# Optimization experiments

Hardware: AMD Instinct MI355X
Metric: run time of the kernel (lower is better)

## Reference

```python
import jax, jax.numpy as jnp
import numpy as np

NUM_HEADS = 16
GROUP_NUM = 4
HIDDEN = 1024
HEAD_DIM = HIDDEN // NUM_HEADS
EPS = 1e-5


def layernorm(x, g, b):
    mu = jnp.mean(x, axis=-1, keepdims=True)
    var = jnp.var(x, axis=-1, keepdims=True)
    return (x - mu) * jax.lax.rsqrt(var + EPS) * g + b


def setup_inputs() -> dict:
    key = jax.random.key(0)
    ks = jax.random.split(key, 12)
    s = 0.02
    return {
        "hidden_state": jax.random.normal(ks[0], (2, 2048, HIDDEN), jnp.float32),
        "wq": jax.random.normal(ks[1], (HIDDEN, HIDDEN), jnp.float32) * s,
        "bq": jnp.zeros((HIDDEN,), jnp.float32),
        "wk": jax.random.normal(ks[2], (GROUP_NUM * HEAD_DIM, HIDDEN), jnp.float32) * s,
        "bk": jnp.zeros((GROUP_NUM * HEAD_DIM,), jnp.float32),
        "wv": jax.random.normal(ks[3], (GROUP_NUM * HEAD_DIM, HIDDEN), jnp.float32) * s,
        "bv": jnp.zeros((GROUP_NUM * HEAD_DIM,), jnp.float32),
        "wo": jax.random.normal(ks[4], (HIDDEN, HIDDEN), jnp.float32) * s,
        "bo": jnp.zeros((HIDDEN,), jnp.float32),
        "ln_g": jnp.ones((HIDDEN,), jnp.float32),
        "ln_b": jnp.zeros((HIDDEN,), jnp.float32),
        "w1": jax.random.normal(ks[5], (HIDDEN, HIDDEN), jnp.float32) * s,
        "b1": jnp.zeros((HIDDEN,), jnp.float32),
        "w2": jax.random.normal(ks[6], (HIDDEN, HIDDEN), jnp.float32) * s,
        "b2": jnp.zeros((HIDDEN,), jnp.float32),
        "fln_g": jnp.ones((HIDDEN,), jnp.float32),
        "fln_b": jnp.zeros((HIDDEN,), jnp.float32),
    }


def reference(hidden_state, wq, bq, wk, bk, wv, bv, wo, bo, ln_g, ln_b,
              w1, b1, w2, b2, fln_g, fln_b):
    B, S, H = hidden_state.shape
    hpg = NUM_HEADS // GROUP_NUM  # heads per KV group

    q = hidden_state @ wq.T + bq  # [B,S,H]
    k = hidden_state @ wk.T + bk  # [B,S,G*D]
    v = hidden_state @ wv.T + bv

    q = q.reshape(B, S, NUM_HEADS, HEAD_DIM).transpose(0, 2, 1, 3)      # [B,Hh,S,D]
    k = k.reshape(B, S, GROUP_NUM, HEAD_DIM).transpose(0, 2, 1, 3)      # [B,G,S,D]
    v = v.reshape(B, S, GROUP_NUM, HEAD_DIM).transpose(0, 2, 1, 3)
    # expand KV groups to full head count (consecutive repeat, matching torch expand+reshape)
    k = jnp.repeat(k, hpg, axis=1)  # [B,Hh,S,D]
    v = jnp.repeat(v, hpg, axis=1)

    scale = 1.0 / jnp.sqrt(jnp.float32(HEAD_DIM))
    scores = jnp.einsum('bhsd,bhtd->bhst', q, k) * scale  # [B,Hh,S,S]
    probs = jax.nn.softmax(scores, axis=-1)
    attn = jnp.einsum('bhst,bhtd->bhsd', probs, v)  # [B,Hh,S,D]

    # Faithful to source: transpose(-1,-2) then raw flat view to [B, S, Hh*D]
    attn = jnp.swapaxes(attn, -1, -2).reshape(B, -1, HEAD_DIM * NUM_HEADS)

    out = layernorm(hidden_state + attn @ wo.T + bo, ln_g, ln_b)
    ffn = out @ w1.T + b1
    ffn = jax.nn.relu(ffn) @ w2.T + b2
    return layernorm(out + ffn, fln_g, fln_b)
```

## Files before the change

### kernel.cpp

```cpp
#include <hip/hip_runtime.h>
#include <math.h>

#define HIDDEN 1024
#define SEQ 2048

typedef __attribute__((ext_vector_type(8))) short short8;
typedef __attribute__((ext_vector_type(4))) float f32x4;

__device__ __forceinline__ unsigned short f2bf(float x) {
  union { float f; unsigned u; } c; c.f = x;
  unsigned r = c.u + 0x7FFFu + ((c.u >> 16) & 1u);
  return (unsigned short)(r >> 16);
}
__device__ __forceinline__ float bf2f(unsigned short h) {
  union { unsigned u; float f; } c; c.u = ((unsigned)h) << 16;
  return c.f;
}

__device__ __forceinline__ void async_copy16(const void* g, void* l) {
  __builtin_amdgcn_global_load_lds(
      (const __attribute__((address_space(1))) unsigned int*)g,
      (__attribute__((address_space(3))) unsigned int*)l, 16, 0, 0);
}

__global__ __launch_bounds__(256) void cvt_all(
    const float* __restrict__ hs, const float* __restrict__ wq,
    const float* __restrict__ wk, const float* __restrict__ wv,
    const float* __restrict__ wo, const float* __restrict__ w1,
    const float* __restrict__ w2,
    unsigned short* __restrict__ hsb, unsigned short* __restrict__ wqb,
    unsigned short* __restrict__ wkb, unsigned short* __restrict__ wvb,
    unsigned short* __restrict__ wob, unsigned short* __restrict__ w1b,
    unsigned short* __restrict__ w2b)
{
  const int i = blockIdx.x * 256 + threadIdx.x;
  const float* src; unsigned short* dst; int off;
  if (i < 1048576)      { src = hs; dst = hsb; off = i; }
  else if (i < 1310720) { src = wq; dst = wqb; off = i - 1048576; }
  else if (i < 1376256) { src = wk; dst = wkb; off = i - 1310720; }
  else if (i < 1441792) { src = wv; dst = wvb; off = i - 1376256; }
  else if (i < 1703936) { src = wo; dst = wob; off = i - 1441792; }
  else if (i < 1966080) { src = w1; dst = w1b; off = i - 1703936; }
  else                  { src = w2; dst = w2b; off = i - 1966080; }
  float4 v = ((const float4*)src)[off];
  ushort4 o;
  o.x = f2bf(v.x); o.y = f2bf(v.y); o.z = f2bf(v.z); o.w = f2bf(v.w);
  ((ushort4*)dst)[off] = o;
}

template<bool RELU>
__global__ __launch_bounds__(256) void gemm_mfma(
    const unsigned short* __restrict__ A, const unsigned short* __restrict__ W,
    const float* __restrict__ bias, unsigned short* __restrict__ C,
    int M, int N, int K)
{
  __shared__ unsigned short As[2][64 * 64];
  __shared__ unsigned short Bs[2][128 * 64];
  const int tid = threadIdx.x;
  const int lane = tid & 63, wave = tid >> 6;
  const int ln = lane & 15, quad = lane >> 4;
  const int wm = (wave >> 1) * 32, wn = (wave & 1) * 64;
  const int m0 = blockIdx.y * 64, n0 = blockIdx.x * 128;

  f32x4 acc[2][4];
#pragma unroll
  for (int i = 0; i < 2; ++i)
#pragma unroll
    for (int j = 0; j < 4; ++j) acc[i][j] = (f32x4){0.f, 0.f, 0.f, 0.f};

  auto stage = [&](int buf, int k0) {
#pragma unroll
    for (int it = 0; it < 2; ++it) {
      const int c = (wave * 2 + it) * 64 + lane;
      const int row = c >> 3, gc = (c & 7) ^ (row & 7);
      async_copy16(A + (size_t)(m0 + row) * K + k0 + gc * 8,
                   &As[buf][(wave * 2 + it) * 512]);
    }
#pragma unroll
    for (int it = 0; it < 4; ++it) {
      const int c = (wave * 4 + it) * 64 + lane;
      const int row = c >> 3, gc = (c & 7) ^ (row & 7);
      async_copy16(W + (size_t)(n0 + row) * K + k0 + gc * 8,
                   &Bs[buf][(wave * 4 + it) * 512]);
    }
  };

  stage(0, 0);
  for (int k0 = 0; k0 < K; k0 += 64) {
    const int buf = (k0 >> 6) & 1;
    __syncthreads();
    if (k0 + 64 < K) stage(buf ^ 1, k0 + 64);

    short8 af[2][2], bfr[4][2];
#pragma unroll
    for (int i = 0; i < 2; ++i) {
      const int row = wm + i * 16 + ln;
#pragma unroll
      for (int f = 0; f < 2; ++f) {
        const int ch = row * 8 + ((f * 4 + quad) ^ (row & 7));
        af[i][f] = *(const short8*)&As[buf][ch * 8];
      }
    }
#pragma unroll
    for (int j = 0; j < 4; ++j) {
      const int row = wn + j * 16 + ln;
#pragma unroll
      for (int f = 0; f < 2; ++f) {
        const int ch = row * 8 + ((f * 4 + quad) ^ (row & 7));
        bfr[j][f] = *(const short8*)&Bs[buf][ch * 8];
      }
    }
#pragma unroll
    for (int i = 0; i < 2; ++i)
#pragma unroll
      for (int j = 0; j < 4; ++j) {
        acc[i][j] = __builtin_amdgcn_mfma_f32_16x16x32_bf16(af[i][0], bfr[j][0], acc[i][j], 0, 0, 0);
        acc[i][j] = __builtin_amdgcn_mfma_f32_16x16x32_bf16(af[i][1], bfr[j][1], acc[i][j], 0, 0, 0);
      }
  }

#pragma unroll
  for (int j = 0; j < 4; ++j) {
    const int n = n0 + wn + j * 16 + ln;
    const float bv = bias[n];
#pragma unroll
    for (int i = 0; i < 2; ++i) {
#pragma unroll
      for (int rr = 0; rr < 4; ++rr) {
        const int m = m0 + wm + i * 16 + quad * 4 + rr;
        float v = acc[i][j][rr] + bv;
        if (RELU) v = fmaxf(v, 0.f);
        C[(size_t)m * N + n] = f2bf(v);
      }
    }
  }
}

__global__ __launch_bounds__(256) void gemm_qkv(
    const unsigned short* __restrict__ A,
    const unsigned short* __restrict__ Wq, const unsigned short* __restrict__ Wk,
    const unsigned short* __restrict__ Wv,
    const float* __restrict__ bq, const float* __restrict__ bk,
    const float* __restrict__ bv,
    unsigned short* __restrict__ Qo, unsigned short* __restrict__ Ko,
    unsigned short* __restrict__ Vt)
{
  __shared__ unsigned short As[2][64 * 64];
  __shared__ unsigned short Bs[2][128 * 64];
  const int bx = blockIdx.x;
  int mode, nw0;
  const unsigned short* W;
  const float* bias;
  if (bx < 8)       { mode = 0; W = Wq; bias = bq; nw0 = bx * 128; }
  else if (bx < 10) { mode = 1; W = Wk; bias = bk; nw0 = (bx - 8) * 128; }
  else              { mode = 2; W = Wv; bias = bv; nw0 = (bx - 10) * 128; }

  const int tid = threadIdx.x;
  const int lane = tid & 63, wave = tid >> 6;
  const int ln = lane & 15, quad = lane >> 4;
  const int wm = (wave >> 1) * 32, wn = (wave & 1) * 64;
  const int m0 = blockIdx.y * 64;
  const int K = 1024;

  f32x4 acc[2][4];
#pragma unroll
  for (int i = 0; i < 2; ++i)
#pragma unroll
    for (int j = 0; j < 4; ++j) acc[i][j] = (f32x4){0.f, 0.f, 0.f, 0.f};

  auto stage = [&](int buf, int k0) {
#pragma unroll
    for (int it = 0; it < 2; ++it) {
      const int c = (wave * 2 + it) * 64 + lane;
      const int row = c >> 3, gc = (c & 7) ^ (row & 7);
      async_copy16(A + (size_t)(m0 + row) * K + k0 + gc * 8,
                   &As[buf][(wave * 2 + it) * 512]);
    }
#pragma unroll
    for (int it = 0; it < 4; ++it) {
      const int c = (wave * 4 + it) * 64 + lane;
      const int row = c >> 3, gc = (c & 7) ^ (row & 7);
      async_copy16(W + (size_t)(nw0 + row) * K + k0 + gc * 8,
                   &Bs[buf][(wave * 4 + it) * 512]);
    }
  };

  stage(0, 0);
  for (int k0 = 0; k0 < K; k0 += 64) {
    const int buf = (k0 >> 6) & 1;
    __syncthreads();
    if (k0 + 64 < K) stage(buf ^ 1, k0 + 64);

    short8 af[2][2], bfr[4][2];
#pragma unroll
    for (int i = 0; i < 2; ++i) {
      const int row = wm + i * 16 + ln;
#pragma unroll
      for (int f = 0; f < 2; ++f) {
        const int ch = row * 8 + ((f * 4 + quad) ^ (row & 7));
        af[i][f] = *(const short8*)&As[buf][ch * 8];
      }
    }
#pragma unroll
    for (int j = 0; j < 4; ++j) {
      const int row = wn + j * 16 + ln;
#pragma unroll
      for (int f = 0; f < 2; ++f) {
        const int ch = row * 8 + ((f * 4 + quad) ^ (row & 7));
        bfr[j][f] = *(const short8*)&Bs[buf][ch * 8];
      }
    }
#pragma unroll
    for (int i = 0; i < 2; ++i)
#pragma unroll
      for (int j = 0; j < 4; ++j) {
        acc[i][j] = __builtin_amdgcn_mfma_f32_16x16x32_bf16(af[i][0], bfr[j][0], acc[i][j], 0, 0, 0);
        acc[i][j] = __builtin_amdgcn_mfma_f32_16x16x32_bf16(af[i][1], bfr[j][1], acc[i][j], 0, 0, 0);
      }
  }

#pragma unroll
  for (int j = 0; j < 4; ++j) {
    const int nl = nw0 + wn + j * 16 + ln;
    const float bvv = bias[nl];
#pragma unroll
    for (int i = 0; i < 2; ++i) {
#pragma unroll
      for (int rr = 0; rr < 4; ++rr) {
        const int m = m0 + wm + i * 16 + quad * 4 + rr;
        const float v = acc[i][j][rr] + bvv;
        if (mode == 0) {
          Qo[(size_t)m * 1024 + nl] = f2bf(v);
        } else if (mode == 1) {
          Ko[(size_t)m * 256 + nl] = f2bf(v);
        } else {
          const int b = m >> 11, s = m & 2047;
          Vt[((size_t)b * 256 + nl) * SEQ + s] = f2bf(v);
        }
      }
    }
  }
}

#define AST 80
__global__ __launch_bounds__(256) void attn_mfma(
    const unsigned short* __restrict__ Q, const unsigned short* __restrict__ Kb,
    const unsigned short* __restrict__ Vt, unsigned short* __restrict__ O)
{
  __shared__ unsigned short Ks[64][AST];
  __shared__ unsigned short Vs[64][AST];
  __shared__ unsigned short Ps[4][16][AST];

  const int bid = blockIdx.x;
  const int qblk = bid & 31, h = (bid >> 5) & 15, b = bid >> 9, g = h >> 2;
  const int tid = threadIdx.x, lane = tid & 63, wave = tid >> 6;
  const int ln = lane & 15, quad = lane >> 4, q8 = quad * 8;
  const int s0 = qblk * 64;
  const float qscale = 0.125f * 1.44269504f;

  {
    const int r = tid >> 2, c16 = (tid & 3) * 16;
    const unsigned short* src = Q + (size_t)(b * SEQ + s0 + r) * 1024 + h * 64 + c16;
#pragma unroll
    for (int hlf = 0; hlf < 2; ++hlf) {
      ushort4 v = *(const ushort4*)(src + hlf * 8);
      ushort4 w = *(const ushort4*)(src + hlf * 8 + 4);
      ushort4 o1, o2;
      o1.x = f2bf(bf2f(v.x) * qscale); o1.y = f2bf(bf2f(v.y) * qscale);
      o1.z = f2bf(bf2f(v.z) * qscale); o1.w = f2bf(bf2f(v.w) * qscale);
      o2.x = f2bf(bf2f(w.x) * qscale); o2.y = f2bf(bf2f(w.y) * qscale);
      o2.z = f2bf(bf2f(w.z) * qscale); o2.w = f2bf(bf2f(w.w) * qscale);
      *(ushort4*)&Ks[r][c16 + hlf * 8] = o1;
      *(ushort4*)&Ks[r][c16 + hlf * 8 + 4] = o2;
    }
  }
  __syncthreads();
  const short8 qf0 = *(const short8*)&Ks[wave * 16 + ln][q8];
  const short8 qf1 = *(const short8*)&Ks[wave * 16 + ln][32 + q8];

  f32x4 of[4];
  float lsum[4] = {0.f, 0.f, 0.f, 0.f};
#pragma unroll
  for (int jd = 0; jd < 4; ++jd) of[jd] = (f32x4){0.f, 0.f, 0.f, 0.f};

  for (int t0 = 0; t0 < SEQ; t0 += 64) {
    __syncthreads();
    {
      const int r = tid >> 2, c8 = (tid & 3) * 8;
      const unsigned short* ksrc = Kb + (size_t)(b * SEQ + t0 + r) * 256 + g * 64;
      const unsigned short* vsrc = Vt + (size_t)(b * 256 + g * 64 + r) * SEQ + t0;
      *(uint4*)&Ks[r][c8]      = *(const uint4*)(ksrc + c8);
      *(uint4*)&Ks[r][c8 + 32] = *(const uint4*)(ksrc + c8 + 32);
      *(uint4*)&Vs[r][c8]      = *(const uint4*)(vsrc + c8);
      *(uint4*)&Vs[r][c8 + 32] = *(const uint4*)(vsrc + c8 + 32);
    }
    __syncthreads();

    f32x4 sc[4];
#pragma unroll
    for (int jn = 0; jn < 4; ++jn) {
      sc[jn] = (f32x4){0.f, 0.f, 0.f, 0.f};
      const short8 kf0 = *(const short8*)&Ks[jn * 16 + ln][q8];
      const short8 kf1 = *(const short8*)&Ks[jn * 16 + ln][32 + q8];
      sc[jn] = __builtin_amdgcn_mfma_f32_16x16x32_bf16(qf0, kf0, sc[jn], 0, 0, 0);
      sc[jn] = __builtin_amdgcn_mfma_f32_16x16x32_bf16(qf1, kf1, sc[jn], 0, 0, 0);
    }

#pragma unroll
    for (int r = 0; r < 4; ++r) {
      const int prow = quad * 4 + r;
      float psum = 0.f;
#pragma unroll
      for (int jn = 0; jn < 4; ++jn) {
        union { float f; unsigned u; } c;
        c.f = exp2f(sc[jn][r]);
        const unsigned hi = c.u & 0xFFFF0000u;
        union { unsigned u; float f; } t; t.u = hi;
        psum += t.f;
        Ps[wave][prow][jn * 16 + ln] = (unsigned short)(hi >> 16);
      }
      lsum[r] += psum;
    }

    const short8 pf0 = *(const short8*)&Ps[wave][ln][q8];
    const short8 pf1 = *(const short8*)&Ps[wave][ln][32 + q8];
#pragma unroll
    for (int jd = 0; jd < 4; ++jd) {
      const short8 vf0 = *(const short8*)&Vs[jd * 16 + ln][q8];
      const short8 vf1 = *(const short8*)&Vs[jd * 16 + ln][32 + q8];
      of[jd] = __builtin_amdgcn_mfma_f32_16x16x32_bf16(pf0, vf0, of[jd], 0, 0, 0);
      of[jd] = __builtin_amdgcn_mfma_f32_16x16x32_bf16(pf1, vf1, of[jd], 0, 0, 0);
    }
  }

#pragma unroll
  for (int r = 0; r < 4; ++r) {
    float s = lsum[r];
    s += __shfl_xor(s, 1);
    s += __shfl_xor(s, 2);
    s += __shfl_xor(s, 4);
    s += __shfl_xor(s, 8);
    lsum[r] = s;
  }

#pragma unroll
  for (int r = 0; r < 4; ++r) {
    const float inv = 1.0f / lsum[r];
    const int s = s0 + wave * 16 + quad * 4 + r;
#pragma unroll
    for (int jd = 0; jd < 4; ++jd) {
      const int d = jd * 16 + ln;
      O[((size_t)b * 1024 + h * 64 + d) * SEQ + s] = f2bf(of[jd][r] * inv);
    }
  }
}

__device__ __forceinline__ void ln_core(float x[4], const float* gam, const float* bet,
                                        int tid, float out[4]) {
  float s1 = x[0] + x[1] + x[2] + x[3];
  float s2 = x[0] * x[0] + x[1] * x[1] + x[2] * x[2] + x[3] * x[3];
#pragma unroll
  for (int off = 1; off < 64; off <<= 1) {
    s1 += __shfl_xor(s1, off);
    s2 += __shfl_xor(s2, off);
  }
  __shared__ float r1[4], r2[4];
  const int wave = tid >> 6;
  if ((tid & 63) == 0) { r1[wave] = s1; r2[wave] = s2; }
  __syncthreads();
  s1 = r1[0] + r1[1] + r1[2] + r1[3];
  s2 = r2[0] + r2[1] + r2[2] + r2[3];
  const float mu  = s1 * (1.0f / HIDDEN);
  const float var = s2 * (1.0f / HIDDEN) - mu * mu;
  const float inv = rsqrtf(var + 1e-5f);
  float4 gv = *(const float4*)&gam[tid * 4];
  float4 bv = *(const float4*)&bet[tid * 4];
  out[0] = (x[0] - mu) * inv * gv.x + bv.x;
  out[1] = (x[1] - mu) * inv * gv.y + bv.y;
  out[2] = (x[2] - mu) * inv * gv.z + bv.z;
  out[3] = (x[3] - mu) * inv * gv.w + bv.w;
}

__global__ __launch_bounds__(256) void resid_ln1(
    const float* __restrict__ X, const unsigned short* __restrict__ Y,
    const float* __restrict__ gam, const float* __restrict__ bet,
    unsigned short* __restrict__ outb)
{
  const int row = blockIdx.x, tid = threadIdx.x;
  const size_t base = (size_t)row * HIDDEN + tid * 4;
  float4 a = *(const float4*)&X[base];
  ushort4 yv = *(const ushort4*)&Y[base];
  float x[4] = {a.x + bf2f(yv.x), a.y + bf2f(yv.y), a.z + bf2f(yv.z), a.w + bf2f(yv.w)};
  float o[4];
  ln_core(x, gam, bet, tid, o);
  ushort4 ov;
  ov.x = f2bf(o[0]); ov.y = f2bf(o[1]); ov.z = f2bf(o[2]); ov.w = f2bf(o[3]);
  *(ushort4*)&outb[base] = ov;
}

__global__ __launch_bounds__(256) void resid_ln2(
    const unsigned short* __restrict__ X, const unsigned short* __restrict__ Y,
    const float* __restrict__ gam, const float* __restrict__ bet,
    float* __restrict__ out)
{
  const int row = blockIdx.x, tid = threadIdx.x;
  const size_t base = (size_t)row * HIDDEN + tid * 4;
  ushort4 xv = *(const ushort4*)&X[base];
  ushort4 yv = *(const ushort4*)&Y[base];
  float x[4] = {bf2f(xv.x) + bf2f(yv.x), bf2f(xv.y) + bf2f(yv.y),
                bf2f(xv.z) + bf2f(yv.z), bf2f(xv.w) + bf2f(yv.w)};
  float o[4];
  ln_core(x, gam, bet, tid, o);
  float4 ov; ov.x = o[0]; ov.y = o[1]; ov.z = o[2]; ov.w = o[3];
  *(float4*)&out[base] = ov;
}

extern "C" void kernel_launch(void* const* d_in, const int* in_sizes, int n_in,
                              void* d_out, int out_size, void* d_ws, size_t ws_size,
                              hipStream_t stream)
{
  (void)in_sizes; (void)n_in; (void)out_size; (void)ws_size;
  const float* hs  = (const float*)d_in[0];
  const float* wq  = (const float*)d_in[1];
  const float* bq  = (const float*)d_in[2];
  const float* wk  = (const float*)d_in[3];
  const float* bk  = (const float*)d_in[4];
  const float* wv  = (const float*)d_in[5];
  const float* bvp = (const float*)d_in[6];
  const float* wo  = (const float*)d_in[7];
  const float* bo  = (const float*)d_in[8];
  const float* lng = (const float*)d_in[9];
  const float* lnb = (const float*)d_in[10];
  const float* w1  = (const float*)d_in[11];
  const float* b1  = (const float*)d_in[12];
  const float* w2  = (const float*)d_in[13];
  const float* b2  = (const float*)d_in[14];
  const float* flg = (const float*)d_in[15];
  const float* flb = (const float*)d_in[16];
  float* out = (float*)d_out;

  unsigned short* w = (unsigned short*)d_ws;
  unsigned short* wqb = w;
  unsigned short* wkb = w + 1048576;
  unsigned short* wvb = w + 1310720;
  unsigned short* wob = w + 1572864;
  unsigned short* w1b = w + 2621440;
  unsigned short* w2b = w + 3670016;
  unsigned short* hsb = w + 4718592;
  unsigned short* qb  = w + 8912896;
  unsigned short* kb  = w + 13107200;
  unsigned short* vt  = w + 14155776;
  unsigned short* att = w + 15204352;
  unsigned short* f1b = hsb;
  unsigned short* yb  = qb;
  unsigned short* obb = att;
  unsigned short* f2b = qb;

  dim3 blk(256);
  cvt_all<<<dim3(8704), blk, 0, stream>>>(hs, wq, wk, wv, wo, w1, w2,
                                          hsb, wqb, wkb, wvb, wob, w1b, w2b);

  gemm_qkv<<<dim3(12, 64), blk, 0, stream>>>(hsb, wqb, wkb, wvb, bq, bk, bvp,
                                             qb, kb, vt);
  attn_mfma<<<dim3(1024), blk, 0, stream>>>(qb, kb, vt, att);
  gemm_mfma<false><<<dim3(8, 64), blk, 0, stream>>>(att, wob, bo, yb, 4096, 1024, 1024);
  resid_ln1<<<dim3(4096), blk, 0, stream>>>(hs, yb, lng, lnb, obb);
  gemm_mfma<true><<<dim3(8, 64), blk, 0, stream>>>(obb, w1b, b1, f1b, 4096, 1024, 1024);
  gemm_mfma<false><<<dim3(8, 64), blk, 0, stream>>>(f1b, w2b, b2, f2b, 4096, 1024, 1024);
  resid_ln2<<<dim3(4096), blk, 0, stream>>>(obb, f2b, flg, flb, out);
}
```

Baseline: 271.7 us.

## Process 32 query rows per wave in attention to reuse K/V tiles

Each attention block now covers 128 query rows instead of 64, with every wave handling two 16-row query sub-tiles. This halves the grid and halves how many times each K/V tile is staged into LDS, and each K/V fragment read from LDS now feeds two MFMAs. Q fragments are loaded straight from global memory into registers and scaled there, so the LDS staging pass and its barrier go away. The cost is more accumulator registers per wave and only 512 blocks, which may lower occupancy and load balance.

```diff
diff --git a/kernel.cpp b/kernel.cpp
--- a/kernel.cpp
+++ b/kernel.cpp
@@ -242,46 +242,43 @@
   }
 }
 
-#define AST 80
 __global__ __launch_bounds__(256) void attn_mfma(
     const unsigned short* __restrict__ Q, const unsigned short* __restrict__ Kb,
     const unsigned short* __restrict__ Vt, unsigned short* __restrict__ O)
 {
-  __shared__ unsigned short Ks[64][AST];
-  __shared__ unsigned short Vs[64][AST];
-  __shared__ unsigned short Ps[4][16][AST];
+  __shared__ unsigned short Ks[64][80];
+  __shared__ unsigned short Vs[64][80];
+  __shared__ unsigned short Ps[4][32][72];
 
   const int bid = blockIdx.x;
-  const int qblk = bid & 31, h = (bid >> 5) & 15, b = bid >> 9, g = h >> 2;
+  const int qblk = bid & 15, h = (bid >> 4) & 15, b = bid >> 8, g = h >> 2;
   const int tid = threadIdx.x, lane = tid & 63, wave = tid >> 6;
   const int ln = lane & 15, quad = lane >> 4, q8 = quad * 8;
-  const int s0 = qblk * 64;
+  const int wq = qblk * 128 + wave * 32;
   const float qscale = 0.125f * 1.44269504f;
 
-  {
-    const int r = tid >> 2, c16 = (tid & 3) * 16;
-    const unsigned short* src = Q + (size_t)(b * SEQ + s0 + r) * 1024 + h * 64 + c16;
-#pragma unroll
-    for (int hlf = 0; hlf < 2; ++hlf) {
-      ushort4 v = *(const ushort4*)(src + hlf * 8);
-      ushort4 w = *(const ushort4*)(src + hlf * 8 + 4);
-      ushort4 o1, o2;
-      o1.x = f2bf(bf2f(v.x) * qscale); o1.y = f2bf(bf2f(v.y) * qscale);
-      o1.z = f2bf(bf2f(v.z) * qscale); o1.w = f2bf(bf2f(v.w) * qscale);
-      o2.x = f2bf(bf2f(w.x) * qscale); o2.y = f2bf(bf2f(w.y) * qscale);
-      o2.z = f2bf(bf2f(w.z) * qscale); o2.w = f2bf(bf2f(w.w) * qscale);
-      *(ushort4*)&Ks[r][c16 + hlf * 8] = o1;
-      *(ushort4*)&Ks[r][c16 + hlf * 8 + 4] = o2;
-    }
-  }
-  __syncthreads();
-  const short8 qf0 = *(const short8*)&Ks[wave * 16 + ln][q8];
-  const short8 qf1 = *(const short8*)&Ks[wave * 16 + ln][32 + q8];
-
-  f32x4 of[4];
-  float lsum[4] = {0.f, 0.f, 0.f, 0.f};
-#pragma unroll
-  for (int jd = 0; jd < 4; ++jd) of[jd] = (f32x4){0.f, 0.f, 0.f, 0.f};
+  short8 qf[2][2];
+#pragma unroll
+  for (int qi = 0; qi < 2; ++qi) {
+    const unsigned short* qsrc =
+        Q + ((size_t)(b * SEQ + wq + qi * 16 + ln)) * 1024 + h * 64 + q8;
+    qf[qi][0] = *(const short8*)qsrc;
+    qf[qi][1] = *(const short8*)(qsrc + 32);
+  }
+#pragma unroll
+  for (int qi = 0; qi < 2; ++qi)
+#pragma unroll
+    for (int hf = 0; hf < 2; ++hf)
+#pragma unroll
+      for (int e = 0; e < 8; ++e)
+        qf[qi][hf][e] = (short)f2bf(bf2f((unsigned short)qf[qi][hf][e]) * qscale);
+
+  f32x4 of[2][4];
+  float lsum[8] = {0.f, 0.f, 0.f, 0.f, 0.f, 0.f, 0.f, 0.f};
+#pragma unroll
+  for (int qi = 0; qi < 2; ++qi)
+#pragma unroll
+    for (int jd = 0; jd < 4; ++jd) of[qi][jd] = (f32x4){0.f, 0.f, 0.f, 0.f};
 
   for (int t0 = 0; t0 < SEQ; t0 += 64) {
     __syncthreads();
@@ -296,63 +293,78 @@
     }
     __syncthreads();
 
-    f32x4 sc[4];
+    f32x4 sc[2][4];
 #pragma unroll
     for (int jn = 0; jn < 4; ++jn) {
-      sc[jn] = (f32x4){0.f, 0.f, 0.f, 0.f};
       const short8 kf0 = *(const short8*)&Ks[jn * 16 + ln][q8];
       const short8 kf1 = *(const short8*)&Ks[jn * 16 + ln][32 + q8];
-      sc[jn] = __builtin_amdgcn_mfma_f32_16x16x32_bf16(qf0, kf0, sc[jn], 0, 0, 0);
-      sc[jn] = __builtin_amdgcn_mfma_f32_16x16x32_bf16(qf1, kf1, sc[jn], 0, 0, 0);
-    }
-
-#pragma unroll
-    for (int r = 0; r < 4; ++r) {
-      const int prow = quad * 4 + r;
-      float psum = 0.f;
-#pragma unroll
-      for (int jn = 0; jn < 4; ++jn) {
-        union { float f; unsigned u; } c;
-        c.f = exp2f(sc[jn][r]);
-        const unsigned hi = c.u & 0xFFFF0000u;
-        union { unsigned u; float f; } t; t.u = hi;
-        psum += t.f;
-        Ps[wave][prow][jn * 16 + ln] = (unsigned short)(hi >> 16);
-      }
-      lsum[r] += psum;
-    }
-
-    const short8 pf0 = *(const short8*)&Ps[wave][ln][q8];
-    const short8 pf1 = *(const short8*)&Ps[wave][ln][32 + q8];
+#pragma unroll
+      for (int qi = 0; qi < 2; ++qi) {
+        f32x4 z = (f32x4){0.f, 0.f, 0.f, 0.f};
+        z = __builtin_amdgcn_mfma_f32_16x16x32_bf16(qf[qi][0], kf0, z, 0, 0, 0);
+        z = __builtin_amdgcn_mfma_f32_16x16x32_bf16(qf[qi][1], kf1, z, 0, 0, 0);
+        sc[qi][jn] = z;
+      }
+    }
+
+#pragma unroll
+    for (int qi = 0; qi < 2; ++qi)
+#pragma unroll
+      for (int r = 0; r < 4; ++r) {
+        const int prow = qi * 16 + quad * 4 + r;
+        float psum = 0.f;
+#pragma unroll
+        for (int jn = 0; jn < 4; ++jn) {
+          union { float f; unsigned u; } c;
+          c.f = exp2f(sc[qi][jn][r]);
+          const unsigned hi = c.u & 0xFFFF0000u;
+          union { unsigned u; float f; } t; t.u = hi;
+          psum += t.f;
+          Ps[wave][prow][jn * 16 + ln] = (unsigned short)(hi >> 16);
+        }
+        lsum[qi * 4 + r] += psum;
+      }
+
+    short8 pf[2][2];
+#pragma unroll
+    for (int qi = 0; qi < 2; ++qi) {
+      pf[qi][0] = *(const short8*)&Ps[wave][qi * 16 + ln][q8];
+      pf[qi][1] = *(const short8*)&Ps[wave][qi * 16 + ln][32 + q8];
+    }
 #pragma unroll
     for (int jd = 0; jd < 4; ++jd) {
       const short8 vf0 = *(const short8*)&Vs[jd * 16 + ln][q8];
       const short8 vf1 = *(const short8*)&Vs[jd * 16 + ln][32 + q8];
-      of[jd] = __builtin_amdgcn_mfma_f32_16x16x32_bf16(pf0, vf0, of[jd], 0, 0, 0);
-      of[jd] = __builtin_amdgcn_mfma_f32_16x16x32_bf16(pf1, vf1, of[jd], 0, 0, 0);
-    }
-  }
-
-#pragma unroll
-  for (int r = 0; r < 4; ++r) {
-    float s = lsum[r];
+#pragma unroll
+      for (int qi = 0; qi < 2; ++qi) {
+        of[qi][jd] = __builtin_amdgcn_mfma_f32_16x16x32_bf16(pf[qi][0], vf0, of[qi][jd], 0, 0, 0);
+        of[qi][jd] = __builtin_amdgcn_mfma_f32_16x16x32_bf16(pf[qi][1], vf1, of[qi][jd], 0, 0, 0);
+      }
+    }
+  }
+
+#pragma unroll
+  for (int i = 0; i < 8; ++i) {
+    float s = lsum[i];
     s += __shfl_xor(s, 1);
     s += __shfl_xor(s, 2);
     s += __shfl_xor(s, 4);
     s += __shfl_xor(s, 8);
-    lsum[r] = s;
-  }
-
-#pragma unroll
-  for (int r = 0; r < 4; ++r) {
-    const float inv = 1.0f / lsum[r];
-    const int s = s0 + wave * 16 + quad * 4 + r;
-#pragma unroll
-    for (int jd = 0; jd < 4; ++jd) {
-      const int d = jd * 16 + ln;
-      O[((size_t)b * 1024 + h * 64 + d) * SEQ + s] = f2bf(of[jd][r] * inv);
-    }
-  }
+    lsum[i] = s;
+  }
+
+#pragma unroll
+  for (int qi = 0; qi < 2; ++qi)
+#pragma unroll
+    for (int r = 0; r < 4; ++r) {
+      const float inv = 1.0f / lsum[qi * 4 + r];
+      const int srow = wq + qi * 16 + quad * 4 + r;
+#pragma unroll
+      for (int jd = 0; jd < 4; ++jd) {
+        const int d = jd * 16 + ln;
+        O[((size_t)b * 1024 + h * 64 + d) * SEQ + srow] = f2bf(of[qi][jd][r] * inv);
+      }
+    }
 }
 
 __device__ __forceinline__ void ln_core(float x[4], const float* gam, const float* bet,
@@ -462,7 +474,7 @@
 
   gemm_qkv<<<dim3(12, 64), blk, 0, stream>>>(hsb, wqb, wkb, wvb, bq, bk, bvp,
                                              qb, kb, vt);
-  attn_mfma<<<dim3(1024), blk, 0, stream>>>(qb, kb, vt, att);
+  attn_mfma<<<dim3(512), blk, 0, stream>>>(qb, kb, vt, att);
   gemm_mfma<false><<<dim3(8, 64), blk, 0, stream>>>(att, wob, bo, yb, 4096, 1024, 1024);
   resid_ln1<<<dim3(4096), blk, 0, stream>>>(hs, yb, lng, lnb, obb);
   gemm_mfma<true><<<dim3(8, 64), blk, 0, stream>>>(obb, w1b, b1, f1b, 4096, 1024, 1024);
```

After: 279.3 us. +2.8%, slower.

## Double-buffer K/V tiles with async LDS copies and XOR-swizzled layout in attention

Applied to the files above, without the earlier changes.

The attention kernel now stages K and V tiles directly into LDS with global_load_lds async copies into two buffers, prefetching the next tile while the current one is being computed. This removes one barrier per iteration. The LDS tiles and the P scratch use an XOR-swizzled 64-wide layout in place of the padded stride, to avoid bank conflicts. Q fragments are loaded straight from global into registers instead of going through LDS, and the output is written as 4-wide vector stores. The risk is that the single barrier is not enough to make the async copies visible before use, since there is no explicit vmcnt wait.

```diff
diff --git a/kernel.cpp b/kernel.cpp
--- a/kernel.cpp
+++ b/kernel.cpp
@@ -242,14 +242,13 @@
   }
 }
 
-#define AST 80
 __global__ __launch_bounds__(256) void attn_mfma(
     const unsigned short* __restrict__ Q, const unsigned short* __restrict__ Kb,
     const unsigned short* __restrict__ Vt, unsigned short* __restrict__ O)
 {
-  __shared__ unsigned short Ks[64][AST];
-  __shared__ unsigned short Vs[64][AST];
-  __shared__ unsigned short Ps[4][16][AST];
+  __shared__ unsigned short Ks[2][64 * 64];
+  __shared__ unsigned short Vs[2][64 * 64];
+  __shared__ unsigned short Ps[4][16 * 64];
 
   const int bid = blockIdx.x;
   const int qblk = bid & 31, h = (bid >> 5) & 15, b = bid >> 9, g = h >> 2;
@@ -258,57 +257,63 @@
   const int s0 = qblk * 64;
   const float qscale = 0.125f * 1.44269504f;
 
+  const int ln7 = ln & 7;
+  const int x0 = (quad ^ ln7) * 8;
+  const int x1 = ((4 + quad) ^ ln7) * 8;
+
+  short8 qf0, qf1;
   {
-    const int r = tid >> 2, c16 = (tid & 3) * 16;
-    const unsigned short* src = Q + (size_t)(b * SEQ + s0 + r) * 1024 + h * 64 + c16;
-#pragma unroll
-    for (int hlf = 0; hlf < 2; ++hlf) {
-      ushort4 v = *(const ushort4*)(src + hlf * 8);
-      ushort4 w = *(const ushort4*)(src + hlf * 8 + 4);
-      ushort4 o1, o2;
-      o1.x = f2bf(bf2f(v.x) * qscale); o1.y = f2bf(bf2f(v.y) * qscale);
-      o1.z = f2bf(bf2f(v.z) * qscale); o1.w = f2bf(bf2f(v.w) * qscale);
-      o2.x = f2bf(bf2f(w.x) * qscale); o2.y = f2bf(bf2f(w.y) * qscale);
-      o2.z = f2bf(bf2f(w.z) * qscale); o2.w = f2bf(bf2f(w.w) * qscale);
-      *(ushort4*)&Ks[r][c16 + hlf * 8] = o1;
-      *(ushort4*)&Ks[r][c16 + hlf * 8 + 4] = o2;
-    }
-  }
-  __syncthreads();
-  const short8 qf0 = *(const short8*)&Ks[wave * 16 + ln][q8];
-  const short8 qf1 = *(const short8*)&Ks[wave * 16 + ln][32 + q8];
+    const unsigned short* qsrc =
+        Q + ((size_t)(b * SEQ + s0 + wave * 16 + ln)) * 1024 + h * 64 + q8;
+    qf0 = *(const short8*)qsrc;
+    qf1 = *(const short8*)(qsrc + 32);
+#pragma unroll
+    for (int e = 0; e < 8; ++e) {
+      qf0[e] = (short)f2bf(bf2f((unsigned short)qf0[e]) * qscale);
+      qf1[e] = (short)f2bf(bf2f((unsigned short)qf1[e]) * qscale);
+    }
+  }
+
+  const int srow = lane >> 3;
+  const int sgcc = (lane & 7) ^ srow;
+  auto stage = [&](int buf, int t0) {
+#pragma unroll
+    for (int it = 0; it < 2; ++it) {
+      const int row = wave * 16 + it * 8 + srow;
+      async_copy16(Kb + (size_t)(b * SEQ + t0 + row) * 256 + g * 64 + sgcc * 8,
+                   &Ks[buf][(wave * 2 + it) * 512]);
+      async_copy16(Vt + (size_t)(b * 256 + g * 64 + row) * SEQ + t0 + sgcc * 8,
+                   &Vs[buf][(wave * 2 + it) * 512]);
+    }
+  };
 
   f32x4 of[4];
   float lsum[4] = {0.f, 0.f, 0.f, 0.f};
 #pragma unroll
   for (int jd = 0; jd < 4; ++jd) of[jd] = (f32x4){0.f, 0.f, 0.f, 0.f};
 
+  stage(0, 0);
   for (int t0 = 0; t0 < SEQ; t0 += 64) {
+    const int buf = (t0 >> 6) & 1;
     __syncthreads();
-    {
-      const int r = tid >> 2, c8 = (tid & 3) * 8;
-      const unsigned short* ksrc = Kb + (size_t)(b * SEQ + t0 + r) * 256 + g * 64;
-      const unsigned short* vsrc = Vt + (size_t)(b * 256 + g * 64 + r) * SEQ + t0;
-      *(uint4*)&Ks[r][c8]      = *(const uint4*)(ksrc + c8);
-      *(uint4*)&Ks[r][c8 + 32] = *(const uint4*)(ksrc + c8 + 32);
-      *(uint4*)&Vs[r][c8]      = *(const uint4*)(vsrc + c8);
-      *(uint4*)&Vs[r][c8 + 32] = *(const uint4*)(vsrc + c8 + 32);
-    }
-    __syncthreads();
+    if (t0 + 64 < SEQ) stage(buf ^ 1, t0 + 64);
 
     f32x4 sc[4];
 #pragma unroll
     for (int jn = 0; jn < 4; ++jn) {
-      sc[jn] = (f32x4){0.f, 0.f, 0.f, 0.f};
-      const short8 kf0 = *(const short8*)&Ks[jn * 16 + ln][q8];
-      const short8 kf1 = *(const short8*)&Ks[jn * 16 + ln][32 + q8];
-      sc[jn] = __builtin_amdgcn_mfma_f32_16x16x32_bf16(qf0, kf0, sc[jn], 0, 0, 0);
-      sc[jn] = __builtin_amdgcn_mfma_f32_16x16x32_bf16(qf1, kf1, sc[jn], 0, 0, 0);
+      const int krow = (jn * 16 + ln) * 64;
+      const short8 kf0 = *(const short8*)&Ks[buf][krow + x0];
+      const short8 kf1 = *(const short8*)&Ks[buf][krow + x1];
+      f32x4 z = (f32x4){0.f, 0.f, 0.f, 0.f};
+      z = __builtin_amdgcn_mfma_f32_16x16x32_bf16(qf0, kf0, z, 0, 0, 0);
+      z = __builtin_amdgcn_mfma_f32_16x16x32_bf16(qf1, kf1, z, 0, 0, 0);
+      sc[jn] = z;
     }
 
 #pragma unroll
     for (int r = 0; r < 4; ++r) {
       const int prow = quad * 4 + r;
+      const int pr7 = prow & 7;
       float psum = 0.f;
 #pragma unroll
       for (int jn = 0; jn < 4; ++jn) {
@@ -317,22 +322,25 @@
         const unsigned hi = c.u & 0xFFFF0000u;
         union { unsigned u; float f; } t; t.u = hi;
         psum += t.f;
-        Ps[wave][prow][jn * 16 + ln] = (unsigned short)(hi >> 16);
+        const int cc = jn * 2 + (ln >> 3);
+        Ps[wave][prow * 64 + ((cc ^ pr7) * 8) + ln7] = (unsigned short)(hi >> 16);
       }
       lsum[r] += psum;
     }
 
-    const short8 pf0 = *(const short8*)&Ps[wave][ln][q8];
-    const short8 pf1 = *(const short8*)&Ps[wave][ln][32 + q8];
+    const short8 pf0 = *(const short8*)&Ps[wave][ln * 64 + x0];
+    const short8 pf1 = *(const short8*)&Ps[wave][ln * 64 + x1];
 #pragma unroll
     for (int jd = 0; jd < 4; ++jd) {
-      const short8 vf0 = *(const short8*)&Vs[jd * 16 + ln][q8];
-      const short8 vf1 = *(const short8*)&Vs[jd * 16 + ln][32 + q8];
+      const int vrow = (jd * 16 + ln) * 64;
+      const short8 vf0 = *(const short8*)&Vs[buf][vrow + x0];
+      const short8 vf1 = *(const short8*)&Vs[buf][vrow + x1];
       of[jd] = __builtin_amdgcn_mfma_f32_16x16x32_bf16(pf0, vf0, of[jd], 0, 0, 0);
       of[jd] = __builtin_amdgcn_mfma_f32_16x16x32_bf16(pf1, vf1, of[jd], 0, 0, 0);
     }
   }
 
+  float inv[4];
 #pragma unroll
   for (int r = 0; r < 4; ++r) {
     float s = lsum[r];
@@ -340,18 +348,19 @@
     s += __shfl_xor(s, 2);
     s += __shfl_xor(s, 4);
     s += __shfl_xor(s, 8);
-    lsum[r] = s;
-  }
-
-#pragma unroll
-  for (int r = 0; r < 4; ++r) {
-    const float inv = 1.0f / lsum[r];
-    const int s = s0 + wave * 16 + quad * 4 + r;
-#pragma unroll
-    for (int jd = 0; jd < 4; ++jd) {
-      const int d = jd * 16 + ln;
-      O[((size_t)b * 1024 + h * 64 + d) * SEQ + s] = f2bf(of[jd][r] * inv);
-    }
+    inv[r] = 1.0f / s;
+  }
+
+  const int sbase = s0 + wave * 16 + quad * 4;
+#pragma unroll
+  for (int jd = 0; jd < 4; ++jd) {
+    const int d = jd * 16 + ln;
+    ushort4 ov;
+    ov.x = f2bf(of[jd][0] * inv[0]);
+    ov.y = f2bf(of[jd][1] * inv[1]);
+    ov.z = f2bf(of[jd][2] * inv[2]);
+    ov.w = f2bf(of[jd][3] * inv[3]);
+    *(ushort4*)&O[((size_t)b * 1024 + h * 64 + d) * SEQ + sbase] = ov;
   }
 }
 
```

Measured after the change: 267.9 us. Within noise of the previous version (-1.4%).
